# Performance work log

Measured on AMD Instinct MI355X. Metric: run time of the kernel, lower is better.

The kernel has to match this reference:

```python
import jax, jax.numpy as jnp
import numpy as np

NUM_BINS = 256


def _histogram(x):
    # x: [B, C, H, W] in [0, 1]
    B, C, H, W = x.shape
    # torch: clamp(x*(nb-1), 0, nb-1).long(); histc over [0, nb-1] with nb bins
    # -> since values are integers in [0, 255], histc == bincount per (b, c) slice
    idx = jnp.clip(x * (NUM_BINS - 1), 0, NUM_BINS - 1).astype(jnp.int32)
    # offset each (b, c) slice into its own segment of the flat histogram
    offsets = jnp.arange(B * C, dtype=jnp.int32)[:, None] * NUM_BINS  # [B*C, 1]
    flat_idx = (idx.reshape(B * C, H * W) + offsets).reshape(-1)
    hist = jnp.zeros(B * C * NUM_BINS, dtype=jnp.float32).at[flat_idx].add(1.0)
    hist = hist.reshape(B, C, NUM_BINS)
    return hist / (H * W)  # normalize=True


def setup_inputs() -> dict:
    key = jax.random.key(0)
    k1, k2 = jax.random.split(key)
    pred = jax.random.uniform(k1, (16, 3, 512, 512), dtype=jnp.float32)
    target = jax.random.uniform(k2, (16, 3, 512, 512), dtype=jnp.float32)
    return {"pred": pred, "target": target}


def reference(pred, target):
    pred_hist = _histogram(pred)
    target_hist = _histogram(target)
    # F.l1_loss default reduction='mean'
    return jnp.mean(jnp.abs(pred_hist - target_hist))
```

## Files before the change

### kernel.cpp

```cpp
#include <hip/hip_runtime.h>

#define NUM_BINS 256
#define BC 48
#define HW 262144
#define CHUNKS 32
#define THREADS 256

typedef float f4 __attribute__((ext_vector_type(4)));

#define PART_ELEMS (BC * CHUNKS * NUM_BINS)

__global__ __launch_bounds__(THREADS) void hist_part_kernel(const float* __restrict__ pred,
                                                            const float* __restrict__ target,
                                                            unsigned int* __restrict__ part,
                                                            unsigned long long* __restrict__ acc,
                                                            unsigned int* __restrict__ cnt) {
    __shared__ unsigned int h[2][NUM_BINS];
    const int t = threadIdx.x;
    h[0][t] = 0u;
    h[1][t] = 0u;
    if (blockIdx.x == 0 && t == 0) {
        *acc = 0ull;
        *cnt = 0u;
    }
    __syncthreads();

    const int slice = blockIdx.x >> 5;
    const int chunk = blockIdx.x & (CHUNKS - 1);
    const int elems_per_block = HW / CHUNKS;
    const int vec_per_block   = elems_per_block / 4;
    const size_t base = (size_t)slice * HW + (size_t)chunk * elems_per_block;
    const f4* __restrict__ p4 = (const f4*)(pred + base);
    const f4* __restrict__ q4 = (const f4*)(target + base);

    #pragma unroll
    for (int it = 0; it < vec_per_block / THREADS; ++it) {
        const int i = it * THREADS + t;
        f4 a = __builtin_nontemporal_load(&p4[i]);
        f4 b = __builtin_nontemporal_load(&q4[i]);
        atomicAdd(&h[0][(int)(a[0] * 255.0f)], 1u);
        atomicAdd(&h[0][(int)(a[1] * 255.0f)], 1u);
        atomicAdd(&h[0][(int)(a[2] * 255.0f)], 1u);
        atomicAdd(&h[0][(int)(a[3] * 255.0f)], 1u);
        atomicAdd(&h[1][(int)(b[0] * 255.0f)], 1u);
        atomicAdd(&h[1][(int)(b[1] * 255.0f)], 1u);
        atomicAdd(&h[1][(int)(b[2] * 255.0f)], 1u);
        atomicAdd(&h[1][(int)(b[3] * 255.0f)], 1u);
    }
    __syncthreads();

    part[((size_t)slice * CHUNKS + chunk) * NUM_BINS + t] = h[0][t] | (h[1][t] << 16);
}

__global__ __launch_bounds__(THREADS) void slice_reduce_kernel(const unsigned int* __restrict__ part,
                                                               unsigned long long* __restrict__ acc,
                                                               unsigned int* __restrict__ cnt,
                                                               float* __restrict__ out) {
    const int s = blockIdx.x;
    const int t = threadIdx.x;
    unsigned int p = 0u, q = 0u;
    #pragma unroll
    for (int c = 0; c < CHUNKS; ++c) {
        unsigned int w = part[((size_t)s * CHUNKS + c) * NUM_BINS + t];
        p += w & 0xFFFFu;
        q += w >> 16;
    }
    unsigned int d = (p > q) ? (p - q) : (q - p);

    __shared__ unsigned int wsum[THREADS / 64];
    for (int off = 32; off > 0; off >>= 1)
        d += __shfl_down(d, off, 64);
    const int wave = t >> 6;
    const int lane = t & 63;
    if (lane == 0) wsum[wave] = d;
    __syncthreads();

    if (t == 0) {
        unsigned int tot = 0u;
        #pragma unroll
        for (int w = 0; w < THREADS / 64; ++w) tot += wsum[w];

        atomicAdd(acc, (unsigned long long)tot);
        __threadfence();
        unsigned int ticket = atomicAdd(cnt, 1u);
        if (ticket == BC - 1) {
            unsigned long long total = atomicAdd(acc, 0ull);
            out[0] = (float)((double)total / ((double)HW * (double)(BC * NUM_BINS)));
        }
    }
}

extern "C" void kernel_launch(void* const* d_in, const int* in_sizes, int n_in,
                              void* d_out, int out_size, void* d_ws, size_t ws_size,
                              hipStream_t stream) {
    const float* pred   = (const float*)d_in[0];
    const float* target = (const float*)d_in[1];
    float* out = (float*)d_out;

    unsigned int* part = (unsigned int*)d_ws;
    unsigned long long* acc = (unsigned long long*)(part + PART_ELEMS);
    unsigned int* cnt = (unsigned int*)(acc + 1);

    hist_part_kernel<<<BC * CHUNKS, THREADS, 0, stream>>>(pred, target, part, acc, cnt);
    slice_reduce_kernel<<<BC, THREADS, 0, stream>>>(part, acc, cnt, out);
}
```

Before: 23.88 us.

## Spread slice reduction across eight blocks per slice with shared-memory partial sums

The second kernel now launches eight blocks per slice, each owning 32 bins. Within a block, eight thread groups each sum four chunk partials, then combine through shared-memory atomics before a 32-lane shuffle reduction. This is meant to cut the per-thread serial loop over 32 chunk partials and fill more CUs in the small reduction kernel. The cost is more global atomics on the accumulator and ticket counter.

```diff
diff --git a/kernel.cpp b/kernel.cpp
--- a/kernel.cpp
+++ b/kernel.cpp
@@ -5,6 +5,7 @@
 #define HW 262144
 #define CHUNKS 32
 #define THREADS 256
+#define RBLK 8
 
 typedef float f4 __attribute__((ext_vector_type(4)));
 
@@ -56,36 +57,43 @@
                                                                unsigned long long* __restrict__ acc,
                                                                unsigned int* __restrict__ cnt,
                                                                float* __restrict__ out) {
-    const int s = blockIdx.x;
-    const int t = threadIdx.x;
+    const int t  = threadIdx.x;
+    const int s  = blockIdx.x >> 3;
+    const int g  = blockIdx.x & (RBLK - 1);
+    const int b  = (g << 5) + (t & 31);
+    const int cg = t >> 5;
+
+    const size_t base = (size_t)s * CHUNKS * NUM_BINS;
     unsigned int p = 0u, q = 0u;
     #pragma unroll
-    for (int c = 0; c < CHUNKS; ++c) {
-        unsigned int w = part[((size_t)s * CHUNKS + c) * NUM_BINS + t];
+    for (int k = 0; k < 4; ++k) {
+        unsigned int w = part[base + (size_t)(cg * 4 + k) * NUM_BINS + b];
         p += w & 0xFFFFu;
         q += w >> 16;
     }
-    unsigned int d = (p > q) ? (p - q) : (q - p);
 
-    __shared__ unsigned int wsum[THREADS / 64];
-    for (int off = 32; off > 0; off >>= 1)
-        d += __shfl_down(d, off, 64);
-    const int wave = t >> 6;
-    const int lane = t & 63;
-    if (lane == 0) wsum[wave] = d;
+    __shared__ unsigned int P[32], Q[32];
+    if (cg == 0) { P[t] = p; Q[t] = q; }
+    __syncthreads();
+    if (cg != 0) {
+        atomicAdd(&P[t & 31], p);
+        atomicAdd(&Q[t & 31], q);
+    }
     __syncthreads();
 
-    if (t == 0) {
-        unsigned int tot = 0u;
-        #pragma unroll
-        for (int w = 0; w < THREADS / 64; ++w) tot += wsum[w];
-
-        atomicAdd(acc, (unsigned long long)tot);
-        __threadfence();
-        unsigned int ticket = atomicAdd(cnt, 1u);
-        if (ticket == BC - 1) {
-            unsigned long long total = atomicAdd(acc, 0ull);
-            out[0] = (float)((double)total / ((double)HW * (double)(BC * NUM_BINS)));
+    if (t < 32) {
+        unsigned int pp = P[t], qq = Q[t];
+        unsigned int d = (pp > qq) ? (pp - qq) : (qq - pp);
+        for (int off = 16; off > 0; off >>= 1)
+            d += __shfl_down(d, off, 32);
+        if (t == 0) {
+            atomicAdd(acc, (unsigned long long)d);
+            __threadfence();
+            unsigned int ticket = atomicAdd(cnt, 1u);
+            if (ticket == BC * RBLK - 1) {
+                unsigned long long total = atomicAdd(acc, 0ull);
+                out[0] = (float)((double)total / ((double)HW * (double)(BC * NUM_BINS)));
+            }
         }
     }
 }
@@ -102,5 +110,5 @@
     unsigned int* cnt = (unsigned int*)(acc + 1);
 
     hist_part_kernel<<<BC * CHUNKS, THREADS, 0, stream>>>(pred, target, part, acc, cnt);
-    slice_reduce_kernel<<<BC, THREADS, 0, stream>>>(part, acc, cnt, out);
+    slice_reduce_kernel<<<BC * RBLK, THREADS, 0, stream>>>(part, acc, cnt, out);
 }
```

Result: slower. 31.17 us (+30.5%).
